# Kernel tuning notes

Measured on AMD Instinct MI355X. Metric: run time of the kernel, lower is better.

Reference implementation:

```python
import jax, jax.numpy as jnp
import numpy as np

IMAGE_C = 1
IMAGE_W = 28
PIXELS_PER_ROW = IMAGE_W * IMAGE_C  # 28

B, T, E = 16, IMAGE_W * IMAGE_W * IMAGE_C, 512  # T = 784
H = 8
D = E // H  # head_dim = 64


def get_2d_causal_bias(T):
    idx = jnp.arange(T)
    i = idx // PIXELS_PER_ROW          # row index
    j = (idx % PIXELS_PER_ROW) // IMAGE_C  # col index
    c = idx % IMAGE_C                  # channel index
    q_i, k_i = i[:, None], i[None, :]
    q_j, k_j = j[:, None], j[None, :]
    q_c, k_c = c[:, None], c[None, :]
    allowed = (k_i < q_i) | ((k_i == q_i) & (k_j < q_j)) | (
        (k_i == q_i) & (k_j == q_j) & (k_c <= q_c))
    bias = jnp.where(allowed, 0.0, -jnp.inf).astype(jnp.float32)
    return bias[None, None]  # [1, 1, T, T]


def setup_inputs() -> dict:
    key = jax.random.key(0)
    ks = jax.random.split(key, 5)
    s = 1.0 / np.sqrt(E)
    return {
        "x": jax.random.normal(ks[0], (B, T, E), dtype=jnp.float32),
        "Wq": jax.random.normal(ks[1], (E, E), dtype=jnp.float32) * s,
        "bq": jnp.zeros((E,), dtype=jnp.float32),
        "Wk": jax.random.normal(ks[2], (E, E), dtype=jnp.float32) * s,
        "bk": jnp.zeros((E,), dtype=jnp.float32),
        "Wv": jax.random.normal(ks[3], (E, E), dtype=jnp.float32) * s,
        "bv": jnp.zeros((E,), dtype=jnp.float32),
        "Wo": jax.random.normal(ks[4], (E, E), dtype=jnp.float32) * s,
        "bo": jnp.zeros((E,), dtype=jnp.float32),
    }


def reference(x, Wq, bq, Wk, bk, Wv, bv, Wo, bo):
    Bx, Tx, Ex = x.shape
    # projections (torch Linear: y = x @ W.T + b; here W stored as [E, E] used directly)
    Q = (x @ Wq + bq).reshape(Bx, Tx, H, D).transpose(0, 2, 1, 3)  # [B,H,T,D]
    K = (x @ Wk + bk).reshape(Bx, Tx, H, D).transpose(0, 2, 1, 3)
    V = (x @ Wv + bv).reshape(Bx, Tx, H, D).transpose(0, 2, 1, 3)
    scores = jnp.einsum("bhqd,bhkd->bhqk", Q, K) / jnp.sqrt(jnp.float32(D))
    scores = scores + get_2d_causal_bias(Tx)
    attn = jax.nn.softmax(scores, axis=-1)
    ctx = jnp.einsum("bhqk,bhkd->bhqd", attn, V)
    ctx = ctx.transpose(0, 2, 1, 3).reshape(Bx, Tx, Ex)
    return ctx @ Wo + bo
```

## Files before the change

### kernel.cpp

```cpp
#include <hip/hip_runtime.h>
#include <hip/hip_bf16.h>

#define BB    16
#define TT    784
#define TPK   832
#define TPQ   896
#define EE    512
#define HH    8
#define DD    64
#define BT    (BB*TT)

typedef short short8 __attribute__((ext_vector_type(8)));
typedef short short4v __attribute__((ext_vector_type(4)));
typedef float floatx4 __attribute__((ext_vector_type(4)));

__device__ __forceinline__ short f2bf(float f) {
    unsigned u = __builtin_bit_cast(unsigned, f);
    u += 0x7FFFu + ((u >> 16) & 1u);
    return (short)(u >> 16);
}

#define ASYNC16(g, l) __builtin_amdgcn_global_load_lds( \
    (const __attribute__((address_space(1))) void*)(g), \
    (__attribute__((address_space(3))) void*)(l), 16, 0, 0)

__global__ void prep_kernel(const float* __restrict__ x, short* __restrict__ xb,
                            const float* __restrict__ Wq, const float* __restrict__ Wk,
                            const float* __restrict__ Wv, short* __restrict__ wqkvt,
                            const float* __restrict__ Wo, short* __restrict__ wot,
                            short* __restrict__ Qb, short* __restrict__ Kb, short* __restrict__ Vt)
{
    __shared__ short t[64][65];
    int b = blockIdx.x;
    if (b < 3136) {
        int i = (b * 256 + threadIdx.x) * 8;
        float4 a = *(const float4*)(x + i);
        float4 c = *(const float4*)(x + i + 4);
        short8 o;
        o[0] = f2bf(a.x); o[1] = f2bf(a.y); o[2] = f2bf(a.z); o[3] = f2bf(a.w);
        o[4] = f2bf(c.x); o[5] = f2bf(c.y); o[6] = f2bf(c.z); o[7] = f2bf(c.w);
        *(short8*)(xb + i) = o;
    } else if (b < 3392) {
        const float* W; short* out; int n0, k0;
        if (b < 3328) {
            int tt = b - 3136;
            n0 = (tt % 24) * 64; k0 = (tt / 24) * 64;
            W = (n0 < 512) ? Wq : (n0 < 1024 ? Wk : Wv);
            out = wqkvt;
        } else {
            int tt = b - 3328;
            n0 = (tt % 8) * 64; k0 = (tt / 8) * 64;
            W = Wo; out = wot;
        }
        int nn0 = n0 & 511;
        for (int i = threadIdx.x; i < 4096; i += 256) {
            int r = i >> 6, c = i & 63;
            t[r][c] = f2bf(W[(k0 + r) * 512 + nn0 + c]);
        }
        __syncthreads();
        for (int i = threadIdx.x; i < 4096; i += 256) {
            int nr = i >> 6, kc = i & 63;
            out[(n0 + nr) * 512 + k0 + kc] = t[kc][nr];
        }
    } else {
        int c = (b - 3392) * 256 + threadIdx.x;
        short8 z = (short8){0,0,0,0,0,0,0,0};
        if (c < 114688) {
            int bh = c / 896, j = c - bh * 896;
            *(short8*)&Qb[(bh * TPQ + TT) * 64 + j * 8] = z;
        } else if (c < 163840) {
            int c2 = c - 114688;
            int bh = c2 / 384, j = c2 - bh * 384;
            *(short8*)&Kb[(bh * TPK + TT) * 64 + j * 8] = z;
        } else {
            int c3 = c - 163840;
            int bh = c3 / 384, j = c3 - bh * 384;
            int d = j / 6, m = j - d * 6;
            *(short8*)&Vt[(bh * 64 + d) * TPK + TT + m * 8] = z;
        }
    }
}

__global__ __launch_bounds__(256, 2) void gemm_qkv_kernel(
    const short* __restrict__ A, const short* __restrict__ Bt,
    const float* __restrict__ bq, const float* __restrict__ bk, const float* __restrict__ bv,
    short* __restrict__ Qb, short* __restrict__ Kb, short* __restrict__ Vt)
{
    __shared__ __align__(16) short smem[24576];
    short* As0 = smem;
    short* Bs0 = smem + 16384;

    const int m0 = blockIdx.x * 256, n0 = blockIdx.y * 128;
    const int tid = threadIdx.x;
    const int lane = tid & 63, w = tid >> 6;
    const int l16 = lane & 15, quad = lane >> 4;

    const short* Ag = A  + (size_t)(m0 + w * 64 + (lane >> 2)) * 512 + (lane & 3) * 8;
    const short* Bg = Bt + (size_t)(n0 + w * 32 + (lane >> 2)) * 512 + (lane & 3) * 8;
    short* Asw = As0 + w * 64 * 32;
    short* Bsw = Bs0 + w * 32 * 32;

    floatx4 acc[4][8];
    #pragma unroll
    for (int i = 0; i < 4; i++)
        #pragma unroll
        for (int j = 0; j < 8; j++)
            acc[i][j] = (floatx4){0.f, 0.f, 0.f, 0.f};

    #pragma unroll
    for (int p = 0; p < 4; p++) ASYNC16(Ag + p * 16 * 512, Asw + p * 512);
    ASYNC16(Bg, Bsw);
    ASYNC16(Bg + 16 * 512, Bsw + 512);

    for (int it = 0; it < 16; it++) {
        __syncthreads();
        if (it < 15) {
            int nb = (it + 1) & 1;
            int ko = (it + 1) * 32;
            #pragma unroll
            for (int p = 0; p < 4; p++)
                ASYNC16(Ag + ko + p * 16 * 512, Asw + nb * 8192 + p * 512);
            ASYNC16(Bg + ko,            Bsw + nb * 4096);
            ASYNC16(Bg + ko + 16 * 512, Bsw + nb * 4096 + 512);
        }
        const short* as = As0 + (it & 1) * 8192;
        const short* bs = Bs0 + (it & 1) * 4096;
        short8 af[4], bf[8];
        #pragma unroll
        for (int i = 0; i < 4; i++)
            af[i] = *(const short8*)&as[(w * 64 + i * 16 + l16) * 32 + quad * 8];
        #pragma unroll
        for (int j = 0; j < 8; j++)
            bf[j] = *(const short8*)&bs[(j * 16 + l16) * 32 + quad * 8];
        #pragma unroll
        for (int mi = 0; mi < 4; mi++)
            #pragma unroll
            for (int ni = 0; ni < 8; ni++)
                acc[mi][ni] = __builtin_amdgcn_mfma_f32_16x16x32_bf16(af[mi], bf[ni], acc[mi][ni], 0, 0, 0);
    }

    const int sel = n0 >> 9;
    if (sel == 2) {
        #pragma unroll
        for (int mi = 0; mi < 4; mi++) {
            int m = m0 + w * 64 + mi * 16 + quad * 4;
            int bb = m / TT, t = m - bb * TT;
            #pragma unroll
            for (int ni = 0; ni < 8; ni++) {
                int nn = (n0 + ni * 16 + l16) & 511;
                int hh = nn >> 6, dd = nn & 63;
                float b = bv[nn];
                short4v pv;
                #pragma unroll
                for (int r = 0; r < 4; r++) pv[r] = f2bf(acc[mi][ni][r] + b);
                *(short4v*)&Vt[((size_t)(bb * HH + hh) * 64 + dd) * TPK + t] = pv;
            }
        }
    } else {
        short* Ct = smem;
        const float* bias = (sel == 0) ? bq : bk;
        short* dst = (sel == 0) ? Qb : Kb;
        const int tp = (sel == 0) ? TPQ : TPK;
        const int nlc = lane * 2;
        const int nnc = (n0 + nlc) & 511;
        const int hhc = nnc >> 6, ddc = nnc & 63;
        #pragma unroll
        for (int h = 0; h < 2; h++) {
            __syncthreads();
            if ((w >> 1) == h) {
                int wl = w & 1;
                #pragma unroll
                for (int mi = 0; mi < 4; mi++) {
                    #pragma unroll
                    for (int ni = 0; ni < 8; ni++) {
                        int nl = ni * 16 + l16;
                        int nn = (n0 + nl) & 511;
                        float b = bias[nn];
                        #pragma unroll
                        for (int r = 0; r < 4; r++) {
                            float v = acc[mi][ni][r] + b;
                            if (sel == 0) v *= 0.125f;
                            Ct[(wl * 64 + mi * 16 + quad * 4 + r) * 130 + nl] = f2bf(v);
                        }
                    }
                }
            }
            __syncthreads();
            #pragma unroll 4
            for (int rr = 0; rr < 32; rr++) {
                int ml = w * 32 + rr;
                int m = m0 + h * 128 + ml;
                int bb = m / TT, t = m - bb * TT;
                unsigned pv = *(const unsigned*)&Ct[ml * 130 + nlc];
                *(unsigned*)&dst[((bb * HH + hhc) * tp + t) * 64 + ddc] = pv;
            }
        }
    }
}

#define LK 72
__global__ __launch_bounds__(256, 3) void attn_kernel(
    const short* __restrict__ Qb, const short* __restrict__ Kb, const short* __restrict__ Vt,
    short* __restrict__ ctx)
{
    const int g = blockIdx.x;
    const int low = g & 7, rest = g >> 3;
    const int qt = 12 - (rest >> 4);
    const int bh = ((rest & 15) << 3) | low;
    const int bb = bh >> 3, hh = bh & 7;
    const int tid = threadIdx.x;
    const int lane = tid & 63, w = tid >> 6;
    const int l16 = lane & 15, quad = lane >> 4;

    __shared__ short Ks[2][64 * LK];
    __shared__ short Vs[2][64 * LK];
    __shared__ short Ps[64 * LK];

    const int srow = tid >> 3;
    const int sc8 = (tid & 7) * 8;
    const short* Kbase = Kb + (size_t)(bh * TPK) * 64;
    const short* Vbase = Vt + (size_t)(bh * 64) * TPK;

    short8 kreg[2], vreg[2];
    auto load_tile = [&](int kt) {
        #pragma unroll
        for (int p = 0; p < 2; p++) {
            int row = srow + p * 32;
            kreg[p] = *(const short8*)(Kbase + (kt * 64 + row) * 64 + sc8);
            vreg[p] = *(const short8*)(Vbase + row * TPK + kt * 64 + sc8);
        }
    };
    auto store_tile = [&](int b) {
        #pragma unroll
        for (int p = 0; p < 2; p++) {
            int row = srow + p * 32;
            *(short8*)&Ks[b][row * LK + sc8] = kreg[p];
            *(short8*)&Vs[b][row * LK + sc8] = vreg[p];
        }
    };

    const short* Qrow = Qb + (size_t)(bh * TPQ + qt * 64 + w * 16 + l16) * 64;
    short8 qa0 = *(const short8*)(Qrow + quad * 8);
    short8 qa1 = *(const short8*)(Qrow + 32 + quad * 8);

    floatx4 accO[4];
    floatx4 accL = (floatx4){0.f, 0.f, 0.f, 0.f};
    #pragma unroll
    for (int dt = 0; dt < 4; dt++) accO[dt] = (floatx4){0.f, 0.f, 0.f, 0.f};

    short8 ones8;
    #pragma unroll
    for (int j = 0; j < 8; j++) ones8[j] = (short)0x3F80;

    const int pswz  = (quad >> 1) * 16;
    const int prswz = ((l16 >> 3) & 1) * 16;
    short* Pw = &Ps[(w * 16 + quad * 4) * LK];

    load_tile(0);
    store_tile(0);

    for (int kt = 0; kt <= qt; kt++) {
        const int cb = kt & 1;
        const bool diag = (kt == qt);
        if (kt < qt) load_tile(kt + 1);
        __syncthreads();

        float p[4][4];
        #pragma unroll
        for (int ni = 0; ni < 4; ni++) {
            if (diag && ni > w) {
                #pragma unroll
                for (int r = 0; r < 4; r++) p[ni][r] = 0.f;
                continue;
            }
            short8 kb0 = *(short8*)&Ks[cb][(ni * 16 + l16) * LK + quad * 8];
            short8 kb1 = *(short8*)&Ks[cb][(ni * 16 + l16) * LK + 32 + quad * 8];
            floatx4 z = (floatx4){0.f, 0.f, 0.f, 0.f};
            z = __builtin_amdgcn_mfma_f32_16x16x32_bf16(qa0, kb0, z, 0, 0, 0);
            z = __builtin_amdgcn_mfma_f32_16x16x32_bf16(qa1, kb1, z, 0, 0, 0);
            if (diag && ni == w) {
                #pragma unroll
                for (int r = 0; r < 4; r++)
                    if (l16 > quad * 4 + r) z[r] = -1e30f;
            }
            #pragma unroll
            for (int r = 0; r < 4; r++) p[ni][r] = __expf(z[r]);
        }

        #pragma unroll
        for (int ni = 0; ni < 4; ni++) {
            int col = (ni * 16 + l16) ^ pswz;
            #pragma unroll
            for (int r = 0; r < 4; r++)
                Pw[r * LK + col] = (short)(__builtin_bit_cast(unsigned, p[ni][r]) >> 16);
        }

        #pragma unroll
        for (int kk = 0; kk < 2; kk++) {
            if (diag && (kk * 32 > w * 16 + 15)) continue;
            short8 pa = *(short8*)&Ps[(w * 16 + l16) * LK + ((kk * 32 + quad * 8) ^ prswz)];
            accL = __builtin_amdgcn_mfma_f32_16x16x32_bf16(pa, ones8, accL, 0, 0, 0);
            #pragma unroll
            for (int dt = 0; dt < 4; dt++) {
                short8 vb = *(short8*)&Vs[cb][(dt * 16 + l16) * LK + kk * 32 + quad * 8];
                accO[dt] = __builtin_amdgcn_mfma_f32_16x16x32_bf16(pa, vb, accO[dt], 0, 0, 0);
            }
        }

        if (kt < qt) store_tile((kt + 1) & 1);
    }

    float inv_l[4];
    #pragma unroll
    for (int r = 0; r < 4; r++) inv_l[r] = 1.f / accL[r];
    #pragma unroll
    for (int dt = 0; dt < 4; dt++)
        #pragma unroll
        for (int r = 0; r < 4; r++) {
            int qg = qt * 64 + w * 16 + quad * 4 + r;
            if (qg < TT)
                ctx[(size_t)(bb * TT + qg) * 512 + hh * 64 + dt * 16 + l16] = f2bf(accO[dt][r] * inv_l[r]);
        }
}

__global__ __launch_bounds__(256, 4) void gemm_out_kernel(
    const short* __restrict__ A, const short* __restrict__ Bt,
    const float* __restrict__ bo, float* __restrict__ out)
{
    __shared__ __align__(16) short smem[16384];
    short* As0 = smem;
    short* Bs0 = smem + 8192;

    const int m0 = blockIdx.x * 128, n0 = blockIdx.y * 128;
    const int tid = threadIdx.x;
    const int lane = tid & 63, w = tid >> 6;
    const int wr = w >> 1, wc = w & 1;
    const int l16 = lane & 15, quad = lane >> 4;

    const short* Ag = A  + (size_t)(m0 + w * 32 + (lane >> 2)) * 512 + (lane & 3) * 8;
    const short* Bg = Bt + (size_t)(n0 + w * 32 + (lane >> 2)) * 512 + (lane & 3) * 8;
    short* Asw = As0 + (w * 32) * 32;
    short* Bsw = Bs0 + (w * 32) * 32;

    floatx4 acc[4][4];
    #pragma unroll
    for (int i = 0; i < 4; i++)
        #pragma unroll
        for (int j = 0; j < 4; j++)
            acc[i][j] = (floatx4){0.f, 0.f, 0.f, 0.f};

    ASYNC16(Ag, Asw);
    ASYNC16(Ag + 16 * 512, Asw + 16 * 32);
    ASYNC16(Bg, Bsw);
    ASYNC16(Bg + 16 * 512, Bsw + 16 * 32);

    for (int it = 0; it < 16; it++) {
        __syncthreads();
        if (it < 15) {
            int nb = (it + 1) & 1;
            int ko = (it + 1) * 32;
            ASYNC16(Ag + ko,            Asw + nb * 4096);
            ASYNC16(Ag + ko + 16 * 512, Asw + nb * 4096 + 16 * 32);
            ASYNC16(Bg + ko,            Bsw + nb * 4096);
            ASYNC16(Bg + ko + 16 * 512, Bsw + nb * 4096 + 16 * 32);
        }
        const short* as = As0 + (it & 1) * 4096;
        const short* bs = Bs0 + (it & 1) * 4096;
        short8 af[4], bf[4];
        #pragma unroll
        for (int i = 0; i < 4; i++) {
            af[i] = *(const short8*)&as[(wr * 64 + i * 16 + l16) * 32 + quad * 8];
            bf[i] = *(const short8*)&bs[(wc * 64 + i * 16 + l16) * 32 + quad * 8];
        }
        #pragma unroll
        for (int mi = 0; mi < 4; mi++)
            #pragma unroll
            for (int ni = 0; ni < 4; ni++)
                acc[mi][ni] = __builtin_amdgcn_mfma_f32_16x16x32_bf16(af[mi], bf[ni], acc[mi][ni], 0, 0, 0);
    }

    #pragma unroll
    for (int mi = 0; mi < 4; mi++) {
        #pragma unroll
        for (int ni = 0; ni < 4; ni++) {
            int n = n0 + wc * 64 + ni * 16 + l16;
            float bias = bo[n];
            #pragma unroll
            for (int r = 0; r < 4; r++) {
                int m = m0 + wr * 64 + mi * 16 + quad * 4 + r;
                out[(size_t)m * 512 + n] = acc[mi][ni][r] + bias;
            }
        }
    }
}

extern "C" void kernel_launch(void* const* d_in, const int* in_sizes, int n_in,
                              void* d_out, int out_size, void* d_ws, size_t ws_size,
                              hipStream_t stream) {
    const float* x  = (const float*)d_in[0];
    const float* Wq = (const float*)d_in[1];
    const float* bq = (const float*)d_in[2];
    const float* Wk = (const float*)d_in[3];
    const float* bk = (const float*)d_in[4];
    const float* Wv = (const float*)d_in[5];
    const float* bv = (const float*)d_in[6];
    const float* Wo = (const float*)d_in[7];
    const float* bo = (const float*)d_in[8];
    float* out = (float*)d_out;

    char* ws = (char*)d_ws;
    size_t off = 0;
    auto alloc = [&](size_t bytes) -> void* {
        void* p = ws + off;
        off += (bytes + 255) & ~(size_t)255;
        return p;
    };
    short* xb    = (short*)alloc((size_t)BT * EE * 2);
    short* wqkvt = (short*)alloc((size_t)1536 * 512 * 2);
    short* wot   = (short*)alloc((size_t)512 * 512 * 2);
    short* Qb    = (short*)alloc((size_t)BB * HH * TPQ * DD * 2);
    short* Kb    = (short*)alloc((size_t)BB * HH * TPK * DD * 2);
    short* Vtb   = (short*)alloc((size_t)BB * HH * DD * TPK * 2);
    short* ctxb  = (short*)alloc((size_t)BT * EE * 2);

    prep_kernel<<<4224, 256, 0, stream>>>(x, xb, Wq, Wk, Wv, wqkvt, Wo, wot, Qb, Kb, Vtb);
    gemm_qkv_kernel<<<dim3(49, 12), 256, 0, stream>>>(xb, wqkvt, bq, bk, bv, Qb, Kb, Vtb);
    attn_kernel<<<1664, 256, 0, stream>>>(Qb, Kb, Vtb, ctxb);
    gemm_out_kernel<<<dim3(98, 4), 256, 0, stream>>>(ctxb, wot, bo, out);
}
```

Before: 172.6 us.

## Replace async global-to-LDS loads with register-staged prefetch and shrink QKV GEMM tile

Both GEMM kernels stop using the global_load_lds builtin. They now load the next K-slice into registers before the barrier and write it to LDS after the MFMA loop, giving a register-staged double buffer. The QKV GEMM tile shrinks from 256x128 to 128x128 with a 2x2 warp layout, doubling the grid and raising the occupancy hint to 4 blocks per CU. The epilogue is simplified to a single LDS staging pass. The intent is better latency hiding and more parallelism, at the cost of extra VGPRs and LDS store instructions.

```diff
diff --git a/kernel.cpp b/kernel.cpp
--- a/kernel.cpp
+++ b/kernel.cpp
@@ -19,10 +19,6 @@
     u += 0x7FFFu + ((u >> 16) & 1u);
     return (short)(u >> 16);
 }
-
-#define ASYNC16(g, l) __builtin_amdgcn_global_load_lds( \
-    (const __attribute__((address_space(1))) void*)(g), \
-    (__attribute__((address_space(3))) void*)(l), 16, 0, 0)
 
 __global__ void prep_kernel(const float* __restrict__ x, short* __restrict__ xb,
                             const float* __restrict__ Wq, const float* __restrict__ Wk,
@@ -81,73 +77,80 @@
     }
 }
 
-__global__ __launch_bounds__(256, 2) void gemm_qkv_kernel(
+__global__ __launch_bounds__(256, 4) void gemm_qkv_kernel(
     const short* __restrict__ A, const short* __restrict__ Bt,
     const float* __restrict__ bq, const float* __restrict__ bk, const float* __restrict__ bv,
     short* __restrict__ Qb, short* __restrict__ Kb, short* __restrict__ Vt)
 {
-    __shared__ __align__(16) short smem[24576];
+    __shared__ __align__(16) short smem[16640];
     short* As0 = smem;
-    short* Bs0 = smem + 16384;
-
-    const int m0 = blockIdx.x * 256, n0 = blockIdx.y * 128;
+    short* Bs0 = smem + 8192;
+
+    const int m0 = blockIdx.x * 128, n0 = blockIdx.y * 128;
     const int tid = threadIdx.x;
     const int lane = tid & 63, w = tid >> 6;
+    const int wr = w >> 1, wc = w & 1;
     const int l16 = lane & 15, quad = lane >> 4;
 
-    const short* Ag = A  + (size_t)(m0 + w * 64 + (lane >> 2)) * 512 + (lane & 3) * 8;
-    const short* Bg = Bt + (size_t)(n0 + w * 32 + (lane >> 2)) * 512 + (lane & 3) * 8;
-    short* Asw = As0 + w * 64 * 32;
-    short* Bsw = Bs0 + w * 32 * 32;
-
-    floatx4 acc[4][8];
+    const int srow = w * 32 + (lane >> 2);
+    const int scol = (lane & 3) * 8;
+    const short* Ag = A  + (size_t)(m0 + srow) * 512 + scol;
+    const short* Bg = Bt + (size_t)(n0 + srow) * 512 + scol;
+    const int soff = srow * 32 + scol;
+
+    short8 areg[2], breg[2];
+    auto load_regs = [&](int it) {
+        int ko = it * 32;
+        areg[0] = *(const short8*)(Ag + ko);
+        areg[1] = *(const short8*)(Ag + ko + 16 * 512);
+        breg[0] = *(const short8*)(Bg + ko);
+        breg[1] = *(const short8*)(Bg + ko + 16 * 512);
+    };
+    auto store_regs = [&](int b) {
+        *(short8*)&As0[b * 4096 + soff]            = areg[0];
+        *(short8*)&As0[b * 4096 + soff + 16 * 32]  = areg[1];
+        *(short8*)&Bs0[b * 4096 + soff]            = breg[0];
+        *(short8*)&Bs0[b * 4096 + soff + 16 * 32]  = breg[1];
+    };
+
+    floatx4 acc[4][4];
     #pragma unroll
     for (int i = 0; i < 4; i++)
         #pragma unroll
-        for (int j = 0; j < 8; j++)
+        for (int j = 0; j < 4; j++)
             acc[i][j] = (floatx4){0.f, 0.f, 0.f, 0.f};
 
-    #pragma unroll
-    for (int p = 0; p < 4; p++) ASYNC16(Ag + p * 16 * 512, Asw + p * 512);
-    ASYNC16(Bg, Bsw);
-    ASYNC16(Bg + 16 * 512, Bsw + 512);
+    load_regs(0);
+    store_regs(0);
 
     for (int it = 0; it < 16; it++) {
-        __syncthreads();
-        if (it < 15) {
-            int nb = (it + 1) & 1;
-            int ko = (it + 1) * 32;
-            #pragma unroll
-            for (int p = 0; p < 4; p++)
-                ASYNC16(Ag + ko + p * 16 * 512, Asw + nb * 8192 + p * 512);
-            ASYNC16(Bg + ko,            Bsw + nb * 4096);
-            ASYNC16(Bg + ko + 16 * 512, Bsw + nb * 4096 + 512);
-        }
-        const short* as = As0 + (it & 1) * 8192;
+        if (it < 15) load_regs(it + 1);
+        __syncthreads();
+        const short* as = As0 + (it & 1) * 4096;
         const short* bs = Bs0 + (it & 1) * 4096;
-        short8 af[4], bf[8];
-        #pragma unroll
-        for (int i = 0; i < 4; i++)
-            af[i] = *(const short8*)&as[(w * 64 + i * 16 + l16) * 32 + quad * 8];
-        #pragma unroll
-        for (int j = 0; j < 8; j++)
-            bf[j] = *(const short8*)&bs[(j * 16 + l16) * 32 + quad * 8];
+        short8 af[4], bf[4];
+        #pragma unroll
+        for (int i = 0; i < 4; i++) {
+            af[i] = *(const short8*)&as[(wr * 64 + i * 16 + l16) * 32 + quad * 8];
+            bf[i] = *(const short8*)&bs[(wc * 64 + i * 16 + l16) * 32 + quad * 8];
+        }
         #pragma unroll
         for (int mi = 0; mi < 4; mi++)
             #pragma unroll
-            for (int ni = 0; ni < 8; ni++)
+            for (int ni = 0; ni < 4; ni++)
                 acc[mi][ni] = __builtin_amdgcn_mfma_f32_16x16x32_bf16(af[mi], bf[ni], acc[mi][ni], 0, 0, 0);
+        if (it < 15) store_regs((it + 1) & 1);
     }
 
     const int sel = n0 >> 9;
     if (sel == 2) {
         #pragma unroll
         for (int mi = 0; mi < 4; mi++) {
-            int m = m0 + w * 64 + mi * 16 + quad * 4;
+            int m = m0 + wr * 64 + mi * 16 + quad * 4;
             int bb = m / TT, t = m - bb * TT;
             #pragma unroll
-            for (int ni = 0; ni < 8; ni++) {
-                int nn = (n0 + ni * 16 + l16) & 511;
+            for (int ni = 0; ni < 4; ni++) {
+                int nn = (n0 + wc * 64 + ni * 16 + l16) & 511;
                 int hh = nn >> 6, dd = nn & 63;
                 float b = bv[nn];
                 short4v pv;
@@ -157,43 +160,37 @@
             }
         }
     } else {
+        __syncthreads();
         short* Ct = smem;
         const float* bias = (sel == 0) ? bq : bk;
+        #pragma unroll
+        for (int mi = 0; mi < 4; mi++) {
+            #pragma unroll
+            for (int ni = 0; ni < 4; ni++) {
+                int nl = wc * 64 + ni * 16 + l16;
+                int nn = (n0 + nl) & 511;
+                float b = bias[nn];
+                #pragma unroll
+                for (int r = 0; r < 4; r++) {
+                    float v = acc[mi][ni][r] + b;
+                    if (sel == 0) v *= 0.125f;
+                    Ct[(wr * 64 + mi * 16 + quad * 4 + r) * 130 + nl] = f2bf(v);
+                }
+            }
+        }
+        __syncthreads();
         short* dst = (sel == 0) ? Qb : Kb;
         const int tp = (sel == 0) ? TPQ : TPK;
-        const int nlc = lane * 2;
-        const int nnc = (n0 + nlc) & 511;
-        const int hhc = nnc >> 6, ddc = nnc & 63;
-        #pragma unroll
-        for (int h = 0; h < 2; h++) {
-            __syncthreads();
-            if ((w >> 1) == h) {
-                int wl = w & 1;
-                #pragma unroll
-                for (int mi = 0; mi < 4; mi++) {
-                    #pragma unroll
-                    for (int ni = 0; ni < 8; ni++) {
-                        int nl = ni * 16 + l16;
-                        int nn = (n0 + nl) & 511;
-                        float b = bias[nn];
-                        #pragma unroll
-                        for (int r = 0; r < 4; r++) {
-                            float v = acc[mi][ni][r] + b;
-                            if (sel == 0) v *= 0.125f;
-                            Ct[(wl * 64 + mi * 16 + quad * 4 + r) * 130 + nl] = f2bf(v);
-                        }
-                    }
-                }
-            }
-            __syncthreads();
-            #pragma unroll 4
-            for (int rr = 0; rr < 32; rr++) {
-                int ml = w * 32 + rr;
-                int m = m0 + h * 128 + ml;
-                int bb = m / TT, t = m - bb * TT;
-                unsigned pv = *(const unsigned*)&Ct[ml * 130 + nlc];
-                *(unsigned*)&dst[((bb * HH + hhc) * tp + t) * 64 + ddc] = pv;
-            }
+        int nl = lane * 2;
+        int nn = (n0 + nl) & 511;
+        int hh = nn >> 6, dd = nn & 63;
+        #pragma unroll 4
+        for (int rr = 0; rr < 32; rr++) {
+            int ml = w * 32 + rr;
+            int m = m0 + ml;
+            int bb = m / TT, t = m - bb * TT;
+            unsigned pv = *(const unsigned*)&Ct[ml * 130 + nl];
+            *(unsigned*)&dst[((bb * HH + hh) * tp + t) * 64 + dd] = pv;
         }
     }
 }
@@ -337,10 +334,26 @@
     const int wr = w >> 1, wc = w & 1;
     const int l16 = lane & 15, quad = lane >> 4;
 
-    const short* Ag = A  + (size_t)(m0 + w * 32 + (lane >> 2)) * 512 + (lane & 3) * 8;
-    const short* Bg = Bt + (size_t)(n0 + w * 32 + (lane >> 2)) * 512 + (lane & 3) * 8;
-    short* Asw = As0 + (w * 32) * 32;
-    short* Bsw = Bs0 + (w * 32) * 32;
+    const int srow = w * 32 + (lane >> 2);
+    const int scol = (lane & 3) * 8;
+    const short* Ag = A  + (size_t)(m0 + srow) * 512 + scol;
+    const short* Bg = Bt + (size_t)(n0 + srow) * 512 + scol;
+    const int soff = srow * 32 + scol;
+
+    short8 areg[2], breg[2];
+    auto load_regs = [&](int it) {
+        int ko = it * 32;
+        areg[0] = *(const short8*)(Ag + ko);
+        areg[1] = *(const short8*)(Ag + ko + 16 * 512);
+        breg[0] = *(const short8*)(Bg + ko);
+        breg[1] = *(const short8*)(Bg + ko + 16 * 512);
+    };
+    auto store_regs = [&](int b) {
+        *(short8*)&As0[b * 4096 + soff]            = areg[0];
+        *(short8*)&As0[b * 4096 + soff + 16 * 32]  = areg[1];
+        *(short8*)&Bs0[b * 4096 + soff]            = breg[0];
+        *(short8*)&Bs0[b * 4096 + soff + 16 * 32]  = breg[1];
+    };
 
     floatx4 acc[4][4];
     #pragma unroll
@@ -349,21 +362,12 @@
         for (int j = 0; j < 4; j++)
             acc[i][j] = (floatx4){0.f, 0.f, 0.f, 0.f};
 
-    ASYNC16(Ag, Asw);
-    ASYNC16(Ag + 16 * 512, Asw + 16 * 32);
-    ASYNC16(Bg, Bsw);
-    ASYNC16(Bg + 16 * 512, Bsw + 16 * 32);
+    load_regs(0);
+    store_regs(0);
 
     for (int it = 0; it < 16; it++) {
-        __syncthreads();
-        if (it < 15) {
-            int nb = (it + 1) & 1;
-            int ko = (it + 1) * 32;
-            ASYNC16(Ag + ko,            Asw + nb * 4096);
-            ASYNC16(Ag + ko + 16 * 512, Asw + nb * 4096 + 16 * 32);
-            ASYNC16(Bg + ko,            Bsw + nb * 4096);
-            ASYNC16(Bg + ko + 16 * 512, Bsw + nb * 4096 + 16 * 32);
-        }
+        if (it < 15) load_regs(it + 1);
+        __syncthreads();
         const short* as = As0 + (it & 1) * 4096;
         const short* bs = Bs0 + (it & 1) * 4096;
         short8 af[4], bf[4];
@@ -377,6 +381,7 @@
             #pragma unroll
             for (int ni = 0; ni < 4; ni++)
                 acc[mi][ni] = __builtin_amdgcn_mfma_f32_16x16x32_bf16(af[mi], bf[ni], acc[mi][ni], 0, 0, 0);
+        if (it < 15) store_regs((it + 1) & 1);
     }
 
     #pragma unroll
@@ -424,7 +429,7 @@
     short* ctxb  = (short*)alloc((size_t)BT * EE * 2);
 
     prep_kernel<<<4224, 256, 0, stream>>>(x, xb, Wq, Wk, Wv, wqkvt, Wo, wot, Qb, Kb, Vtb);
-    gemm_qkv_kernel<<<dim3(49, 12), 256, 0, stream>>>(xb, wqkvt, bq, bk, bv, Qb, Kb, Vtb);
+    gemm_qkv_kernel<<<dim3(98, 12), 256, 0, stream>>>(xb, wqkvt, bq, bk, bv, Qb, Kb, Vtb);
     attn_kernel<<<1664, 256, 0, stream>>>(Qb, Kb, Vtb, ctxb);
     gemm_out_kernel<<<dim3(98, 4), 256, 0, stream>>>(ctxb, wot, bo, out);
 }
```

Measured after the change: 165.3 us. 4.2% less time.
